# Kernel optimization log

Measured on AMD Instinct MI355X. Metric: run time of the kernel, lower is better.

Reference implementation:

```python
import jax, jax.numpy as jnp
import numpy as np

SELF_OBS_DIM = 18
NEIGHBOR_OBS_DIM = 6
HIDDEN = 256
NUM_NEIGHBORS = 6
BATCH = 131072


def setup_inputs() -> dict:
    key = jax.random.key(0)
    k1, k2, k3, k4, k5, k6 = jax.random.split(key, 6)
    obs_dim = SELF_OBS_DIM + NEIGHBOR_OBS_DIM * NUM_NEIGHBORS
    self_obs = jax.random.normal(k1, (BATCH, SELF_OBS_DIM), dtype=jnp.float32)
    obs = jax.random.normal(k2, (BATCH, obs_dim), dtype=jnp.float32)
    # MLP params (PyTorch Linear default init scale ~ 1/sqrt(fan_in))
    W1 = jax.random.uniform(k3, (NEIGHBOR_OBS_DIM, HIDDEN), minval=-1.0, maxval=1.0) / np.sqrt(NEIGHBOR_OBS_DIM)
    b1 = jax.random.uniform(k4, (HIDDEN,), minval=-1.0, maxval=1.0) / np.sqrt(NEIGHBOR_OBS_DIM)
    W2 = jax.random.uniform(k5, (HIDDEN, HIDDEN), minval=-1.0, maxval=1.0) / np.sqrt(HIDDEN)
    b2 = jax.random.uniform(k6, (HIDDEN,), minval=-1.0, maxval=1.0) / np.sqrt(HIDDEN)
    return {
        "self_obs": self_obs,
        "obs": obs,
        "W1": W1.astype(jnp.float32),
        "b1": b1.astype(jnp.float32),
        "W2": W2.astype(jnp.float32),
        "b2": b2.astype(jnp.float32),
        "all_neighbor_obs_size": NEIGHBOR_OBS_DIM * NUM_NEIGHBORS,
        "batch_size": BATCH,
    }


def reference(self_obs, obs, W1, b1, W2, b2, all_neighbor_obs_size, batch_size):
    # slice out neighbor observations: obs[:, self_obs_dim : self_obs_dim + all_neighbor_obs_size]
    obs_neighbors = obs[:, SELF_OBS_DIM:SELF_OBS_DIM + all_neighbor_obs_size]
    # reshape to per-neighbor rows: [B * num_neighbors, neighbor_obs_dim]
    x = obs_neighbors.reshape(-1, NEIGHBOR_OBS_DIM)
    # shared 2-layer MLP with tanh (sample-factory default nonlinearity)
    h = jnp.tanh(x @ W1 + b1)
    h = jnp.tanh(h @ W2 + b2)
    # [B, num_neighbors, hidden] -> mean over neighbor axis
    neighbor_embeds = h.reshape(batch_size, -1, HIDDEN)
    mean_embed = jnp.mean(neighbor_embeds, axis=1)
    return mean_embed
```

## Files before the change

### kernel.cpp

```cpp
#include <hip/hip_runtime.h>


#define HID     256
#define OBSD    54
#define SELFD   18
#define TILE_B  8
#define TILE_R  48
#define LDA     264
#define LDH     54
#define BATCHN  131072
#define NTILES  (BATCHN / TILE_B)
#define GRID_WG 2048
#define TANH_K  2.8853900817779268f

typedef __attribute__((ext_vector_type(8))) short bf16x8;
typedef __attribute__((ext_vector_type(4))) float f32x4;

__device__ __forceinline__ unsigned cvt_pk_bf16(float lo, float hi) {
    unsigned r;
    asm("v_cvt_pk_bf16_f32 %0, %1, %2" : "=v"(r) : "v"(lo), "v"(hi));
    return r;
}

__device__ __forceinline__ float tanh_fused(float x, float bK) {
    float t = __builtin_amdgcn_exp2f(__builtin_fmaf(x, TANH_K, bK));
    return 1.0f - 2.0f * __builtin_amdgcn_rcpf(t + 1.0f);
}

__device__ __forceinline__ unsigned bfbits(float f) {
    unsigned u = __float_as_uint(f);
    u += 0x7fffu + ((u >> 16) & 1u);
    return u >> 16;
}

__global__ void prep(const float* __restrict__ W1, const float* __restrict__ W2,
                     short* __restrict__ w1t, short* __restrict__ w2t) {
    int idx = blockIdx.x * 256 + threadIdx.x;
    if (idx < 65536) {
        int n = idx >> 8, k = idx & 255;
        w2t[idx] = (short)bfbits(W2[k * HID + n]);
    } else {
        int j = idx - 65536;
        int n = j >> 5, k = j & 31;
        w1t[j] = (k < 6) ? (short)bfbits(W1[k * HID + n]) : (short)0;
    }
}

__global__ __launch_bounds__(512, 4) void qenc_main(
        const float* __restrict__ obs,
        const short* __restrict__ w1t,
        const float* __restrict__ b1,
        const short* __restrict__ w2t,
        const float* __restrict__ b2,
        float* __restrict__ out)
{
    __shared__ union {
        short a[TILE_R * LDA];
        short ht[HID * LDH];
    } u;

    const int tid  = threadIdx.x;
    const int wave = tid >> 6;
    const int lane = tid & 63;
    const int q    = lane >> 4;
    const int c16  = lane & 15;
    const int colbase = wave * 32;

    bf16x8 Bf[8][2];
    #pragma unroll
    for (int kk = 0; kk < 8; ++kk)
        #pragma unroll
        for (int ct = 0; ct < 2; ++ct)
            Bf[kk][ct] = *(const bf16x8*)
                (w2t + (colbase + ct * 16 + c16) * HID + kk * 32 + q * 8);

    bf16x8 B1f[2];
    #pragma unroll
    for (int ct = 0; ct < 2; ++ct)
        B1f[ct] = *(const bf16x8*)(w1t + (colbase + ct * 16 + c16) * 32 + q * 8);

    float b1s[2][4];
    #pragma unroll
    for (int ct = 0; ct < 2; ++ct)
        #pragma unroll
        for (int g = 0; g < 4; ++g)
            b1s[ct][g] = b1[colbase + ct * 16 + q * 4 + g] * TANH_K;
    float b2s[2];
    #pragma unroll
    for (int ct = 0; ct < 2; ++ct)
        b2s[ct] = b2[colbase + ct * 16 + c16] * TANH_K;

    int soff[3];
    #pragma unroll
    for (int rt = 0; rt < 3; ++rt) {
        int row = rt * 16 + c16;
        soff[rt] = (row / 6) * OBSD + SELFD + (row % 6) * 6;
    }

    for (int tile = blockIdx.x; tile < NTILES; tile += GRID_WG) {
        const size_t obase = (size_t)tile * (TILE_B * OBSD);

        #pragma unroll
        for (int rt = 0; rt < 3; ++rt) {
            const float* src = obs + obase + soff[rt];
            float2 f0 = *(const float2*)(src);
            float2 f1 = *(const float2*)(src + 2);
            float2 f2 = *(const float2*)(src + 4);
            union { unsigned w[4]; bf16x8 v; } xf;
            xf.w[0] = cvt_pk_bf16(f0.x, f0.y);
            xf.w[1] = cvt_pk_bf16(f1.x, f1.y);
            xf.w[2] = cvt_pk_bf16(f2.x, f2.y);
            xf.w[3] = 0u;
            #pragma unroll
            for (int ct = 0; ct < 2; ++ct) {
                f32x4 c = __builtin_amdgcn_mfma_f32_16x16x32_bf16(
                    B1f[ct], xf.v, (f32x4){0.f, 0.f, 0.f, 0.f}, 0, 0, 0);
                float t0 = tanh_fused(c[0], b1s[ct][0]);
                float t1 = tanh_fused(c[1], b1s[ct][1]);
                float t2 = tanh_fused(c[2], b1s[ct][2]);
                float t3 = tanh_fused(c[3], b1s[ct][3]);
                uint2 dd;
                dd.x = cvt_pk_bf16(t0, t1);
                dd.y = cvt_pk_bf16(t2, t3);
                *(uint2*)&u.a[(rt * 16 + c16) * LDA + colbase + ct * 16 + q * 4] = dd;
            }
        }
        __syncthreads();

        f32x4 acc[3][2];
        #pragma unroll
        for (int rt = 0; rt < 3; ++rt)
            #pragma unroll
            for (int ct = 0; ct < 2; ++ct) acc[rt][ct] = (f32x4){0.f, 0.f, 0.f, 0.f};

        #pragma unroll
        for (int kk = 0; kk < 8; ++kk) {
            bf16x8 Af[3];
            #pragma unroll
            for (int rt = 0; rt < 3; ++rt)
                Af[rt] = *(const bf16x8*)&u.a[(rt * 16 + c16) * LDA + kk * 32 + q * 8];
            #pragma unroll
            for (int rt = 0; rt < 3; ++rt)
                #pragma unroll
                for (int ct = 0; ct < 2; ++ct)
                    acc[rt][ct] = __builtin_amdgcn_mfma_f32_16x16x32_bf16(
                        Af[rt], Bf[kk][ct], acc[rt][ct], 0, 0, 0);
        }
        __syncthreads();

        #pragma unroll
        for (int ct = 0; ct < 2; ++ct) {
            const int col = colbase + ct * 16 + c16;
            #pragma unroll
            for (int rt = 0; rt < 3; ++rt) {
                float t0 = tanh_fused(acc[rt][ct][0], b2s[ct]);
                float t1 = tanh_fused(acc[rt][ct][1], b2s[ct]);
                float t2 = tanh_fused(acc[rt][ct][2], b2s[ct]);
                float t3 = tanh_fused(acc[rt][ct][3], b2s[ct]);
                const int row = rt * 16 + q * 4;
                *(unsigned*)&u.ht[col * LDH + row]     = cvt_pk_bf16(t0, t1);
                *(unsigned*)&u.ht[col * LDH + row + 2] = cvt_pk_bf16(t2, t3);
            }
        }

        const int b0 = tile * TILE_B;
        {
            const int col = colbase + (lane & 31);
            const int bl0 = (lane >> 5) * 4;
            #pragma unroll
            for (int jj = 0; jj < 4; ++jj) {
                const int bl = bl0 + jj;
                const unsigned* p = (const unsigned*)&u.ht[col * LDH + bl * 6];
                float s = 0.f;
                #pragma unroll
                for (int d = 0; d < 3; ++d) {
                    unsigned uu = p[d];
                    s += __uint_as_float(uu << 16) + __uint_as_float(uu & 0xffff0000u);
                }
                out[(size_t)(b0 + bl) * HID + col] = s * (1.0f / 6.0f);
            }
        }
        __syncthreads();
    }
}

extern "C" void kernel_launch(void* const* d_in, const int* in_sizes, int n_in,
                              void* d_out, int out_size, void* d_ws, size_t ws_size,
                              hipStream_t stream) {
    const float* obs = (const float*)d_in[1];
    const float* W1  = (const float*)d_in[2];
    const float* b1  = (const float*)d_in[3];
    const float* W2  = (const float*)d_in[4];
    const float* b2  = (const float*)d_in[5];
    float* outp = (float*)d_out;

    short* w2t = (short*)d_ws;
    short* w1t = (short*)((char*)d_ws + 131072);

    prep<<<288, 256, 0, stream>>>(W1, W2, w1t, w2t);
    qenc_main<<<GRID_WG, 512, 0, stream>>>(obs, w1t, b1, w2t, b2, outp);
}
```

Measured before the change: 337.7 us.

## Reduce neighbor mean in registers with cross-lane shuffles instead of LDS transpose

Replaces the LDS round-trip (writing bf16 tanh outputs transposed to shared memory, then re-reading to sum six neighbors) with an in-register reduction. Partial sums over each lane's four MFMA accumulator rows are combined across quads with two xor-shuffles, and each lane writes two batch rows directly. This removes a __syncthreads, the LDS union, and the bf16 quantization of second-layer outputs. In exchange it adds select logic, and the output stores become strided per lane rather than coalesced across 32 consecutive columns.

```diff
diff --git a/kernel.cpp b/kernel.cpp
--- a/kernel.cpp
+++ b/kernel.cpp
@@ -7,7 +7,6 @@
 #define TILE_B  8
 #define TILE_R  48
 #define LDA     264
-#define LDH     54
 #define BATCHN  131072
 #define NTILES  (BATCHN / TILE_B)
 #define GRID_WG 2048
@@ -54,10 +53,7 @@
         const float* __restrict__ b2,
         float* __restrict__ out)
 {
-    __shared__ union {
-        short a[TILE_R * LDA];
-        short ht[HID * LDH];
-    } u;
+    __shared__ short a[TILE_R * LDA];
 
     const int tid  = threadIdx.x;
     const int wave = tid >> 6;
@@ -97,6 +93,10 @@
         soff[rt] = (row / 6) * OBSD + SELFD + (row % 6) * 6;
     }
 
+    const int blA = 2 * q + (q & 1);
+    const int blB = (q < 2) ? (q + 5) : (q - 1);
+    const bool isq0 = (q == 0), isq1 = (q == 1), isq2 = (q == 2);
+
     for (int tile = blockIdx.x; tile < NTILES; tile += GRID_WG) {
         const size_t obase = (size_t)tile * (TILE_B * OBSD);
 
@@ -122,7 +122,7 @@
                 uint2 dd;
                 dd.x = cvt_pk_bf16(t0, t1);
                 dd.y = cvt_pk_bf16(t2, t3);
-                *(uint2*)&u.a[(rt * 16 + c16) * LDA + colbase + ct * 16 + q * 4] = dd;
+                *(uint2*)&a[(rt * 16 + c16) * LDA + colbase + ct * 16 + q * 4] = dd;
             }
         }
         __syncthreads();
@@ -138,7 +138,7 @@
             bf16x8 Af[3];
             #pragma unroll
             for (int rt = 0; rt < 3; ++rt)
-                Af[rt] = *(const bf16x8*)&u.a[(rt * 16 + c16) * LDA + kk * 32 + q * 8];
+                Af[rt] = *(const bf16x8*)&a[(rt * 16 + c16) * LDA + kk * 32 + q * 8];
             #pragma unroll
             for (int rt = 0; rt < 3; ++rt)
                 #pragma unroll
@@ -146,39 +146,32 @@
                     acc[rt][ct] = __builtin_amdgcn_mfma_f32_16x16x32_bf16(
                         Af[rt], Bf[kk][ct], acc[rt][ct], 0, 0, 0);
         }
-        __syncthreads();
 
+        const int b0 = tile * TILE_B;
         #pragma unroll
         for (int ct = 0; ct < 2; ++ct) {
             const int col = colbase + ct * 16 + c16;
+            float s[3], uu[3], f[3];
             #pragma unroll
             for (int rt = 0; rt < 3; ++rt) {
                 float t0 = tanh_fused(acc[rt][ct][0], b2s[ct]);
                 float t1 = tanh_fused(acc[rt][ct][1], b2s[ct]);
                 float t2 = tanh_fused(acc[rt][ct][2], b2s[ct]);
                 float t3 = tanh_fused(acc[rt][ct][3], b2s[ct]);
-                const int row = rt * 16 + q * 4;
-                *(unsigned*)&u.ht[col * LDH + row]     = cvt_pk_bf16(t0, t1);
-                *(unsigned*)&u.ht[col * LDH + row + 2] = cvt_pk_bf16(t2, t3);
+                s[rt] = t0 + t1; uu[rt] = t2 + t3; f[rt] = s[rt] + uu[rt];
             }
-        }
-
-        const int b0 = tile * TILE_B;
-        {
-            const int col = colbase + (lane & 31);
-            const int bl0 = (lane >> 5) * 4;
-            #pragma unroll
-            for (int jj = 0; jj < 4; ++jj) {
-                const int bl = bl0 + jj;
-                const unsigned* p = (const unsigned*)&u.ht[col * LDH + bl * 6];
-                float s = 0.f;
-                #pragma unroll
-                for (int d = 0; d < 3; ++d) {
-                    unsigned uu = p[d];
-                    s += __uint_as_float(uu << 16) + __uint_as_float(uu & 0xffff0000u);
-                }
-                out[(size_t)(b0 + bl) * HID + col] = s * (1.0f / 6.0f);
-            }
+            float A = isq1 ? s[0] : f[0];
+            float B = isq1 ? uu[0] : (isq2 ? f[1] : s[1]);
+            float C = isq2 ? s[2] : (isq1 ? f[1] : uu[1]);
+            float D = isq2 ? uu[2] : f[2];
+            float p1 = isq0 ? C : (isq1 ? A : (isq2 ? D : B));
+            float p2 = (q < 2) ? B : C;
+            float r1 = __shfl_xor(p1, 16);
+            float r2 = __shfl_xor(p2, 48);
+            float own1 = (isq0 ? A : (isq1 ? C : (isq2 ? B : D))) + r1;
+            float own2 = ((q < 2) ? D : A) + r2;
+            out[(size_t)(b0 + blA) * HID + col] = own1 * (1.0f / 6.0f);
+            out[(size_t)(b0 + blB) * HID + col] = own2 * (1.0f / 6.0f);
         }
         __syncthreads();
     }
```

Result: no change. 335.1 us (-0.8%).
